# Kernel tuning notes

Measured on AMD Instinct MI355X. Metric: run time of the kernel, lower is better.

The kernel has to match this reference:

```python
import jax, jax.numpy as jnp
import numpy as np

B = 16384
D = 1024          # entity_dim
N_LAYERS = 4
TEMPERATURE = 32.0  # sqrt(entity_dim)


def setup_inputs() -> dict:
    key = jax.random.key(0)
    ks = jax.random.split(key, 6)
    d2 = 2 * D
    scale = 1.0 / np.sqrt(d2)
    x1 = jax.random.normal(ks[0], (B, D), dtype=jnp.float32)
    x2 = jax.random.normal(ks[1], (B, D), dtype=jnp.float32)
    # stacked per-layer Linear(2D, 2D) params; torch Linear stores W as [out, in]
    Ws = jax.random.normal(ks[2], (N_LAYERS, d2, d2), dtype=jnp.float32) * scale
    bs = jax.random.normal(ks[3], (N_LAYERS, d2), dtype=jnp.float32) * scale
    W_last = jax.random.normal(ks[4], (D, d2), dtype=jnp.float32) * scale
    b_last = jax.random.normal(ks[5], (D,), dtype=jnp.float32) * scale
    return {"x1": x1, "x2": x2, "Ws": Ws, "bs": bs, "W_last": W_last, "b_last": b_last}


def reference(x1, x2, Ws, bs, W_last, b_last):
    # x: [B, 2, D]
    x = jnp.stack((x1, x2), axis=1)
    # attn: [B, 2, 2] -- tiny self-attention over the 2 tokens
    attn = jnp.einsum('bsd,btd->bst', x / TEMPERATURE, x)
    attn = jax.nn.softmax(attn, axis=-1)  # dropout = identity in eval mode
    x = jnp.einsum('bst,btd->bsd', attn, x)
    # concat the two attended tokens -> [B, 2D]
    h = jnp.concatenate((x[:, 0, :], x[:, 1, :]), axis=-1)
    for i in range(N_LAYERS):
        h = jax.nn.relu(h @ Ws[i].T + bs[i])
    return h @ W_last.T + b_last
```

## Files before the change

kernel.cpp:

```cpp
#include <hip/hip_runtime.h>

typedef __bf16 bf16x8 __attribute__((ext_vector_type(8)));
typedef float f32x4 __attribute__((ext_vector_type(4)));

__device__ __forceinline__ unsigned short f2bf(float f) {
    unsigned int u = __builtin_bit_cast(unsigned int, f);
    u += 0x7FFFu + ((u >> 16) & 1u);
    return (unsigned short)(u >> 16);
}

__global__ void cvt_kernel(const float* __restrict__ in,
                           unsigned short* __restrict__ out, long n4) {
    long i = (long)blockIdx.x * blockDim.x + threadIdx.x;
    long stride = (long)gridDim.x * blockDim.x;
    for (; i < n4; i += stride) {
        float4 v = ((const float4*)in)[i];
        ushort4 o;
        o.x = f2bf(v.x); o.y = f2bf(v.y); o.z = f2bf(v.z); o.w = f2bf(v.w);
        ((ushort4*)out)[i] = o;
    }
}

__global__ __launch_bounds__(256) void attn_kernel(
    const float* __restrict__ x1, const float* __restrict__ x2,
    unsigned short* __restrict__ h) {
    const int D = 1024;
    const int lane = threadIdx.x & 63;
    const int wave = threadIdx.x >> 6;
    const long row = (long)blockIdx.x * 4 + wave;
    const float4* p1 = (const float4*)(x1 + row * D);
    const float4* p2 = (const float4*)(x2 + row * D);
    float4 v1[4], v2[4];
    float s11 = 0.f, s12 = 0.f, s22 = 0.f;
#pragma unroll
    for (int j = 0; j < 4; ++j) {
        v1[j] = p1[lane + 64 * j];
        v2[j] = p2[lane + 64 * j];
        s11 += v1[j].x * v1[j].x + v1[j].y * v1[j].y + v1[j].z * v1[j].z + v1[j].w * v1[j].w;
        s12 += v1[j].x * v2[j].x + v1[j].y * v2[j].y + v1[j].z * v2[j].z + v1[j].w * v2[j].w;
        s22 += v2[j].x * v2[j].x + v2[j].y * v2[j].y + v2[j].z * v2[j].z + v2[j].w * v2[j].w;
    }
#pragma unroll
    for (int off = 1; off < 64; off <<= 1) {
        s11 += __shfl_xor(s11, off);
        s12 += __shfl_xor(s12, off);
        s22 += __shfl_xor(s22, off);
    }
    const float a00 = 1.f / (1.f + expf((s12 - s11) * (1.f / 32.f)));
    const float a10 = 1.f / (1.f + expf((s22 - s12) * (1.f / 32.f)));
    const float a01 = 1.f - a00, a11 = 1.f - a10;
    unsigned short* h0 = h + row * 2048;
#pragma unroll
    for (int j = 0; j < 4; ++j) {
        const int f = lane + 64 * j;
        ushort4 o0, o1;
        o0.x = f2bf(a00 * v1[j].x + a01 * v2[j].x);
        o0.y = f2bf(a00 * v1[j].y + a01 * v2[j].y);
        o0.z = f2bf(a00 * v1[j].z + a01 * v2[j].z);
        o0.w = f2bf(a00 * v1[j].w + a01 * v2[j].w);
        o1.x = f2bf(a10 * v1[j].x + a11 * v2[j].x);
        o1.y = f2bf(a10 * v1[j].y + a11 * v2[j].y);
        o1.z = f2bf(a10 * v1[j].z + a11 * v2[j].z);
        o1.w = f2bf(a10 * v1[j].w + a11 * v2[j].w);
        ((ushort4*)(h0))[f] = o0;
        ((ushort4*)(h0 + 1024))[f] = o1;
    }
}

#define BAR   __builtin_amdgcn_s_barrier()
#define LGKM0 asm volatile("s_waitcnt lgkmcnt(0)" ::: "memory")
#define PRIO1 __builtin_amdgcn_s_setprio(1)
#define PRIO0 __builtin_amdgcn_s_setprio(0)

#define MM8(mi0, A00, A01, mi1, A10, A11)                                                        \
  _Pragma("unroll") for (int n = 0; n < 4; ++n) {                                                \
    acc[mi0][n] = __builtin_amdgcn_mfma_f32_16x16x32_bf16(A00, Bf[n][0], acc[mi0][n], 0, 0, 0);  \
    acc[mi0][n] = __builtin_amdgcn_mfma_f32_16x16x32_bf16(A01, Bf[n][1], acc[mi0][n], 0, 0, 0);  \
    acc[mi1][n] = __builtin_amdgcn_mfma_f32_16x16x32_bf16(A10, Bf[n][0], acc[mi1][n], 0, 0, 0);  \
    acc[mi1][n] = __builtin_amdgcn_mfma_f32_16x16x32_bf16(A11, Bf[n][1], acc[mi1][n], 0, 0, 0);  \
  }

template <bool RELU, typename OT>
__global__ __launch_bounds__(512, 2) void gemm256(
    const unsigned short* __restrict__ A,
    const unsigned short* __restrict__ Bw,
    const float* __restrict__ bias,
    OT* __restrict__ C,
    int N, int K) {
    __shared__ unsigned short lds[65536];
    const int tid = threadIdx.x;
    const int lane = tid & 63, wave = tid >> 6;
    const int wm = wave >> 2, wn = wave & 3;
    const int fr = lane & 15, fq = lane >> 4;

    const int cpx = (int)gridDim.x >> 3;
    const int swz = ((int)blockIdx.x & 7) * cpx + ((int)blockIdx.x >> 3);
    const int bm = swz & 63;
    const int bn = swz >> 6;
    const long m0 = (long)bm * 256, n0 = (long)bn * 256;

    const int x0 = fq ^ (fr & 7);
    const int lane_base = fr * 128 + x0 * 16;
    const int aBase = wm * 16384 + lane_base;
    const int bBase = 32768 + (wn >> 1) * 16384 + (wn & 1) * 8192 + lane_base;
    const char* ldsc = (const char*)lds;

    const int l3 = lane >> 3, l7 = lane & 7;
    const long rowb = (long)K * 2;
    const long lane_src = (long)l3 * rowb + ((l7 ^ l3) << 4);
    const char* Abl = (const char*)A + m0 * rowb + lane_src;
    const char* Bbl = (const char*)Bw + n0 * rowb + lane_src;

    auto stage = [&](const char* mb, int matOff, int hf, int kt, int T) {
#pragma unroll
        for (int r = 0; r < 2; ++r) {
            const int W = r * 8 + wave;
            const char* src = mb + (long)(hf * 128 + W * 8) * rowb + kt * 128;
            __builtin_amdgcn_global_load_lds(
                (const __attribute__((address_space(1))) void*)src,
                (__attribute__((address_space(3))) void*)((char*)lds +
                    (T * 65536 + matOff + hf * 16384 + W * 1024)),
                16, 0, 0);
        }
    };

    f32x4 acc[8][4] = {};
    bf16x8 Bf[4][2], A0f[2][2], AL[6][2];

    auto readP1 = [&](int boff) {
#pragma unroll
        for (int n = 0; n < 4; ++n) {
            Bf[n][0] = *(const bf16x8*)(ldsc + boff + bBase + n * 2048);
            Bf[n][1] = *(const bf16x8*)(ldsc + boff + (bBase ^ 64) + n * 2048);
        }
#pragma unroll
        for (int m = 0; m < 2; ++m) {
            A0f[m][0] = *(const bf16x8*)(ldsc + boff + aBase + m * 2048);
            A0f[m][1] = *(const bf16x8*)(ldsc + boff + (aBase ^ 64) + m * 2048);
        }
    };
    auto readP2 = [&](int boff) {
#pragma unroll
        for (int m = 0; m < 6; ++m) {
            AL[m][0] = *(const bf16x8*)(ldsc + boff + aBase + (m + 2) * 2048);
            AL[m][1] = *(const bf16x8*)(ldsc + boff + (aBase ^ 64) + (m + 2) * 2048);
        }
    };

    stage(Abl, 0,     0, 0, 0); stage(Abl, 0,     1, 0, 0);
    stage(Bbl, 32768, 0, 0, 0); stage(Bbl, 32768, 1, 0, 0);
    stage(Abl, 0,     0, 1, 1); stage(Abl, 0,     1, 1, 1);
    asm volatile("s_waitcnt vmcnt(4)" ::: "memory");
    BAR;

    const int NT = K >> 6;
    const int NIT = NT >> 1;
    for (int i = 0; i < NIT; ++i) {
        const int t1 = 2 * i + 1, t2 = t1 + 1, t3 = t1 + 2;
        const bool g = (i + 1 < NIT);

        readP1(0);
        stage(Bbl, 32768, 0, t1, 1);
        BAR; LGKM0; PRIO1;
        MM8(0, A0f[0][0], A0f[0][1], 1, A0f[1][0], A0f[1][1]);
        PRIO0; BAR;

        readP2(0);
        stage(Bbl, 32768, 1, t1, 1);
        BAR; LGKM0; PRIO1;
        MM8(2, AL[0][0], AL[0][1], 3, AL[1][0], AL[1][1]);
        PRIO0; BAR;

        if (g) stage(Abl, 0, 0, t2, 0);
        BAR; PRIO1;
        MM8(4, AL[2][0], AL[2][1], 5, AL[3][0], AL[3][1]);
        PRIO0; BAR;

        if (g) stage(Abl, 0, 1, t2, 0);
        BAR; PRIO1;
        MM8(6, AL[4][0], AL[4][1], 7, AL[5][0], AL[5][1]);
        PRIO0;
        if (g) { asm volatile("s_waitcnt vmcnt(4)" ::: "memory"); }
        else   { asm volatile("s_waitcnt vmcnt(0)" ::: "memory"); }
        BAR;

        readP1(65536);
        if (g) stage(Bbl, 32768, 0, t2, 0);
        BAR; LGKM0; PRIO1;
        MM8(0, A0f[0][0], A0f[0][1], 1, A0f[1][0], A0f[1][1]);
        PRIO0; BAR;

        readP2(65536);
        if (g) stage(Bbl, 32768, 1, t2, 0);
        BAR; LGKM0; PRIO1;
        MM8(2, AL[0][0], AL[0][1], 3, AL[1][0], AL[1][1]);
        PRIO0; BAR;

        if (g) stage(Abl, 0, 0, t3, 1);
        BAR; PRIO1;
        MM8(4, AL[2][0], AL[2][1], 5, AL[3][0], AL[3][1]);
        PRIO0; BAR;

        if (g) stage(Abl, 0, 1, t3, 1);
        BAR; PRIO1;
        MM8(6, AL[4][0], AL[4][1], 7, AL[5][0], AL[5][1]);
        PRIO0;
        if (g) { asm volatile("s_waitcnt vmcnt(4)" ::: "memory"); }
        else   { asm volatile("s_waitcnt vmcnt(0)" ::: "memory"); }
        BAR;
    }

    const long crow0 = m0 + wm * 128 + fq * 4;
    const long ccol0 = n0 + wn * 64 + fr;
#pragma unroll
    for (int n = 0; n < 4; ++n) {
        const float bv = bias[ccol0 + n * 16];
#pragma unroll
        for (int m = 0; m < 8; ++m) {
#pragma unroll
            for (int r = 0; r < 4; ++r) {
                float v = acc[m][n][r] + bv;
                if (RELU) v = v > 0.f ? v : 0.f;
                OT* p = C + (crow0 + m * 16 + r) * N + (ccol0 + n * 16);
                if constexpr (sizeof(OT) == 2) *p = (OT)f2bf(v);
                else *p = v;
            }
        }
    }
}

extern "C" void kernel_launch(void* const* d_in, const int* in_sizes, int n_in,
                              void* d_out, int out_size, void* d_ws, size_t ws_size,
                              hipStream_t stream) {
    const float* x1 = (const float*)d_in[0];
    const float* x2 = (const float*)d_in[1];
    const float* Ws = (const float*)d_in[2];
    const float* bs = (const float*)d_in[3];
    const float* Wl = (const float*)d_in[4];
    const float* bl = (const float*)d_in[5];
    float* out = (float*)d_out;

    char* ws = (char*)d_ws;
    unsigned short* hA  = (unsigned short*)(ws);
    unsigned short* hB  = (unsigned short*)(ws + (67108864L));
    unsigned short* Wbf = (unsigned short*)(ws + (134217728L));
    unsigned short* Wlb = (unsigned short*)(ws + (167772160L));

    cvt_kernel<<<2048, 256, 0, stream>>>(Ws, Wbf, 4L * 2048 * 2048 / 4);
    cvt_kernel<<<512, 256, 0, stream>>>(Wl, Wlb, 1024L * 2048 / 4);

    attn_kernel<<<16384 / 4, 256, 0, stream>>>(x1, x2, hA);

    gemm256<true, unsigned short><<<512, 512, 0, stream>>>(hA, Wbf + 0L * 2048 * 2048, bs + 0 * 2048, hB, 2048, 2048);
    gemm256<true, unsigned short><<<512, 512, 0, stream>>>(hB, Wbf + 1L * 2048 * 2048, bs + 1 * 2048, hA, 2048, 2048);
    gemm256<true, unsigned short><<<512, 512, 0, stream>>>(hA, Wbf + 2L * 2048 * 2048, bs + 2 * 2048, hB, 2048, 2048);
    gemm256<true, unsigned short><<<512, 512, 0, stream>>>(hB, Wbf + 3L * 2048 * 2048, bs + 3 * 2048, hA, 2048, 2048);
    gemm256<false, float><<<256, 512, 0, stream>>>(hA, Wlb, bl, out, 1024, 2048);
}
```

Before: 665.5 us.

## Swap MFMA operands for vectorized epilogue stores and restructure LDS read phases

```diff
diff --git a/kernel.cpp b/kernel.cpp
--- a/kernel.cpp
+++ b/kernel.cpp
@@ -69,16 +69,15 @@
 
 #define BAR   __builtin_amdgcn_s_barrier()
 #define LGKM0 asm volatile("s_waitcnt lgkmcnt(0)" ::: "memory")
+#define VMW(n) asm volatile("s_waitcnt vmcnt(" #n ")" ::: "memory")
 #define PRIO1 __builtin_amdgcn_s_setprio(1)
 #define PRIO0 __builtin_amdgcn_s_setprio(0)
 
-#define MM8(mi0, A00, A01, mi1, A10, A11)                                                        \
-  _Pragma("unroll") for (int n = 0; n < 4; ++n) {                                                \
-    acc[mi0][n] = __builtin_amdgcn_mfma_f32_16x16x32_bf16(A00, Bf[n][0], acc[mi0][n], 0, 0, 0);  \
-    acc[mi0][n] = __builtin_amdgcn_mfma_f32_16x16x32_bf16(A01, Bf[n][1], acc[mi0][n], 0, 0, 0);  \
-    acc[mi1][n] = __builtin_amdgcn_mfma_f32_16x16x32_bf16(A10, Bf[n][0], acc[mi1][n], 0, 0, 0);  \
-    acc[mi1][n] = __builtin_amdgcn_mfma_f32_16x16x32_bf16(A11, Bf[n][1], acc[mi1][n], 0, 0, 0);  \
-  }
+#define MMQ(mb, kk)                                                            \
+  _Pragma("unroll") for (int n = 0; n < 4; ++n)                                \
+  _Pragma("unroll") for (int mq = 0; mq < 4; ++mq)                             \
+    acc[(mb) + mq][n] = __builtin_amdgcn_mfma_f32_16x16x32_bf16(               \
+        Bf[n][kk], Af[mq][kk], acc[(mb) + mq][n], 0, 0, 0);
 
 template <bool RELU, typename OT>
 __global__ __launch_bounds__(512, 2) void gemm256(
@@ -87,7 +86,7 @@
     const float* __restrict__ bias,
     OT* __restrict__ C,
     int N, int K) {
-    __shared__ unsigned short lds[65536];
+    __shared__ __align__(16) unsigned short lds[65536];
     const int tid = threadIdx.x;
     const int lane = tid & 63, wave = tid >> 6;
     const int wm = wave >> 2, wn = wave & 3;
@@ -125,32 +124,29 @@
     };
 
     f32x4 acc[8][4] = {};
-    bf16x8 Bf[4][2], A0f[2][2], AL[6][2];
-
-    auto readP1 = [&](int boff) {
-#pragma unroll
-        for (int n = 0; n < 4; ++n) {
-            Bf[n][0] = *(const bf16x8*)(ldsc + boff + bBase + n * 2048);
-            Bf[n][1] = *(const bf16x8*)(ldsc + boff + (bBase ^ 64) + n * 2048);
-        }
-#pragma unroll
-        for (int m = 0; m < 2; ++m) {
-            A0f[m][0] = *(const bf16x8*)(ldsc + boff + aBase + m * 2048);
-            A0f[m][1] = *(const bf16x8*)(ldsc + boff + (aBase ^ 64) + m * 2048);
-        }
+    bf16x8 Bf[4][2], Af[4][2];
+
+    auto readBA = [&](int boff, int kk) {
+        const int x = kk * 64;
+#pragma unroll
+        for (int n = 0; n < 4; ++n)
+            Bf[n][kk] = *(const bf16x8*)(ldsc + boff + (bBase ^ x) + n * 2048);
+#pragma unroll
+        for (int m = 0; m < 4; ++m)
+            Af[m][kk] = *(const bf16x8*)(ldsc + boff + (aBase ^ x) + m * 2048);
     };
-    auto readP2 = [&](int boff) {
-#pragma unroll
-        for (int m = 0; m < 6; ++m) {
-            AL[m][0] = *(const bf16x8*)(ldsc + boff + aBase + (m + 2) * 2048);
-            AL[m][1] = *(const bf16x8*)(ldsc + boff + (aBase ^ 64) + (m + 2) * 2048);
+    auto readAH = [&](int boff) {
+#pragma unroll
+        for (int m = 0; m < 4; ++m) {
+            Af[m][0] = *(const bf16x8*)(ldsc + boff + aBase + (m + 4) * 2048);
+            Af[m][1] = *(const bf16x8*)(ldsc + boff + (aBase ^ 64) + (m + 4) * 2048);
         }
     };
 
     stage(Abl, 0,     0, 0, 0); stage(Abl, 0,     1, 0, 0);
     stage(Bbl, 32768, 0, 0, 0); stage(Bbl, 32768, 1, 0, 0);
     stage(Abl, 0,     0, 1, 1); stage(Abl, 0,     1, 1, 1);
-    asm volatile("s_waitcnt vmcnt(4)" ::: "memory");
+    VMW(4);
     BAR;
 
     const int NT = K >> 6;
@@ -159,71 +155,59 @@
         const int t1 = 2 * i + 1, t2 = t1 + 1, t3 = t1 + 2;
         const bool g = (i + 1 < NIT);
 
-        readP1(0);
-        stage(Bbl, 32768, 0, t1, 1);
-        BAR; LGKM0; PRIO1;
-        MM8(0, A0f[0][0], A0f[0][1], 1, A0f[1][0], A0f[1][1]);
-        PRIO0; BAR;
-
-        readP2(0);
-        stage(Bbl, 32768, 1, t1, 1);
-        BAR; LGKM0; PRIO1;
-        MM8(2, AL[0][0], AL[0][1], 3, AL[1][0], AL[1][1]);
-        PRIO0; BAR;
-
-        if (g) stage(Abl, 0, 0, t2, 0);
-        BAR; PRIO1;
-        MM8(4, AL[2][0], AL[2][1], 5, AL[3][0], AL[3][1]);
-        PRIO0; BAR;
-
-        if (g) stage(Abl, 0, 1, t2, 0);
-        BAR; PRIO1;
-        MM8(6, AL[4][0], AL[4][1], 7, AL[5][0], AL[5][1]);
-        PRIO0;
-        if (g) { asm volatile("s_waitcnt vmcnt(4)" ::: "memory"); }
-        else   { asm volatile("s_waitcnt vmcnt(0)" ::: "memory"); }
+        readBA(0, 0);
+        stage(Bbl, 32768, 0, t1, 1); stage(Bbl, 32768, 1, t1, 1);
+        BAR; PRIO1; MMQ(0, 0); PRIO0; BAR;
+        readBA(0, 1);
+        BAR; PRIO1; MMQ(0, 1); PRIO0; BAR;
+        readAH(0);
+        LGKM0;
+        BAR; PRIO1; MMQ(4, 0); PRIO0; BAR;
+        if (g) { stage(Abl, 0, 0, t2, 0); stage(Abl, 0, 1, t2, 0); }
+        BAR; PRIO1; MMQ(4, 1); PRIO0;
+        if (g) { VMW(4); } else { VMW(0); }
         BAR;
 
-        readP1(65536);
-        if (g) stage(Bbl, 32768, 0, t2, 0);
-        BAR; LGKM0; PRIO1;
-        MM8(0, A0f[0][0], A0f[0][1], 1, A0f[1][0], A0f[1][1]);
-        PRIO0; BAR;
-
-        readP2(65536);
-        if (g) stage(Bbl, 32768, 1, t2, 0);
-        BAR; LGKM0; PRIO1;
-        MM8(2, AL[0][0], AL[0][1], 3, AL[1][0], AL[1][1]);
-        PRIO0; BAR;
-
-        if (g) stage(Abl, 0, 0, t3, 1);
-        BAR; PRIO1;
-        MM8(4, AL[2][0], AL[2][1], 5, AL[3][0], AL[3][1]);
-        PRIO0; BAR;
-
-        if (g) stage(Abl, 0, 1, t3, 1);
-        BAR; PRIO1;
-        MM8(6, AL[4][0], AL[4][1], 7, AL[5][0], AL[5][1]);
-        PRIO0;
-        if (g) { asm volatile("s_waitcnt vmcnt(4)" ::: "memory"); }
-        else   { asm volatile("s_waitcnt vmcnt(0)" ::: "memory"); }
+        readBA(65536, 0);
+        if (g) { stage(Bbl, 32768, 0, t2, 0); stage(Bbl, 32768, 1, t2, 0); }
+        BAR; PRIO1; MMQ(0, 0); PRIO0; BAR;
+        readBA(65536, 1);
+        BAR; PRIO1; MMQ(0, 1); PRIO0; BAR;
+        readAH(65536);
+        LGKM0;
+        BAR; PRIO1; MMQ(4, 0); PRIO0; BAR;
+        if (g) { stage(Abl, 0, 0, t3, 1); stage(Abl, 0, 1, t3, 1); }
+        BAR; PRIO1; MMQ(4, 1); PRIO0;
+        if (g) { VMW(4); } else { VMW(0); }
         BAR;
     }
 
-    const long crow0 = m0 + wm * 128 + fq * 4;
-    const long ccol0 = n0 + wn * 64 + fr;
-#pragma unroll
-    for (int n = 0; n < 4; ++n) {
-        const float bv = bias[ccol0 + n * 16];
-#pragma unroll
-        for (int m = 0; m < 8; ++m) {
-#pragma unroll
-            for (int r = 0; r < 4; ++r) {
-                float v = acc[m][n][r] + bv;
-                if (RELU) v = v > 0.f ? v : 0.f;
-                OT* p = C + (crow0 + m * 16 + r) * N + (ccol0 + n * 16);
-                if constexpr (sizeof(OT) == 2) *p = (OT)f2bf(v);
-                else *p = v;
+    const long crow0 = m0 + wm * 128 + fr;
+    const long ccol0 = n0 + wn * 64 + fq * 4;
+    float4 bv[4];
+#pragma unroll
+    for (int n = 0; n < 4; ++n) bv[n] = *(const float4*)(bias + ccol0 + n * 16);
+#pragma unroll
+    for (int m = 0; m < 8; ++m) {
+        const long rb = (crow0 + m * 16) * N;
+#pragma unroll
+        for (int n = 0; n < 4; ++n) {
+            float v0 = acc[m][n][0] + bv[n].x;
+            float v1 = acc[m][n][1] + bv[n].y;
+            float v2 = acc[m][n][2] + bv[n].z;
+            float v3 = acc[m][n][3] + bv[n].w;
+            if (RELU) {
+                v0 = v0 > 0.f ? v0 : 0.f; v1 = v1 > 0.f ? v1 : 0.f;
+                v2 = v2 > 0.f ? v2 : 0.f; v3 = v3 > 0.f ? v3 : 0.f;
+            }
+            if constexpr (sizeof(OT) == 2) {
+                uint2 o;
+                o.x = (unsigned)f2bf(v0) | ((unsigned)f2bf(v1) << 16);
+                o.y = (unsigned)f2bf(v2) | ((unsigned)f2bf(v3) << 16);
+                *(uint2*)((unsigned short*)C + rb + ccol0 + n * 16) = o;
+            } else {
+                *(float4*)((float*)C + rb + ccol0 + n * 16) =
+                    make_float4(v0, v1, v2, v3);
             }
         }
     }
```

Result: no change. 662.4 us (-0.5%).
